# Optimization experiments

Hardware: AMD Instinct MI355X
Metric: run time of the kernel (lower is better)

## Reference

```python
import jax, jax.numpy as jnp
import numpy as np

B, N, F, F_, H = 4, 2048, 64, 64, 4
EDGE_PROB = 0.01  # sparsity of the random adjacency


def setup_inputs() -> dict:
    key = jax.random.key(0)
    k_x, k_a, k_ws, k_wn, k_as, k_an = jax.random.split(key, 6)
    X = jax.random.normal(k_x, (B, N, F), dtype=jnp.float32)
    # binary adjacency with self-loops (float, as in the torch module)
    A = (jax.random.uniform(k_a, (B, N, N)) < EDGE_PROB).astype(jnp.float32)
    A = jnp.maximum(A, jnp.eye(N, dtype=jnp.float32)[None, :, :])
    # glorot-uniform-like init scale for [F, F_] kernels
    lim_k = np.sqrt(6.0 / (F + F_)).astype(np.float32)
    lim_a = np.sqrt(6.0 / (F_ + 1)).astype(np.float32)
    W_self = jax.random.uniform(k_ws, (H, F, F_), minval=-lim_k, maxval=lim_k, dtype=jnp.float32)
    W_neigh = jax.random.uniform(k_wn, (H, F, F_), minval=-lim_k, maxval=lim_k, dtype=jnp.float32)
    a_self = jax.random.uniform(k_as, (H, F_), minval=-lim_a, maxval=lim_a, dtype=jnp.float32)
    a_neigh = jax.random.uniform(k_an, (H, F_), minval=-lim_a, maxval=lim_a, dtype=jnp.float32)
    return {"X": X, "A": A, "W_self": W_self, "W_neigh": W_neigh,
            "a_self": a_self, "a_neigh": a_neigh}


def reference(X, A, W_self, W_neigh, a_self, a_neigh):
    # per-head linear projections: [B,H,N,F_]
    feat_self = jnp.einsum('bnf,hfe->bhne', X, W_self)
    feat_neigh = jnp.einsum('bnf,hfe->bhne', X, W_neigh)
    # scalar attention logits per node: [B,H,N]
    s_self = jnp.einsum('bhne,he->bhn', feat_self, a_self)
    s_neigh = jnp.einsum('bhne,he->bhn', feat_neigh, a_neigh)
    # pairwise logits: att[b,h,i,j] = s_self[b,h,i] + s_neigh[b,h,j]
    att = s_self[:, :, :, None] + s_neigh[:, :, None, :]
    att = jax.nn.leaky_relu(att, negative_slope=0.2)
    att = att + (-1e16) * (1.0 - A[:, None, :, :])  # additive adjacency mask
    att = jax.nn.sigmoid(att)
    att_sum = jnp.sum(att, axis=-1, keepdims=True)      # [B,H,N,1]
    inv = 1.0 / (1.0 + att_sum)
    att = att * inv                                      # sigmoid-normalized
    beta_promoter = inv
    # aggregate: self contribution scaled by beta + neighbor aggregation
    node_feat = feat_self * beta_promoter + jnp.einsum('bhnm,bhme->bhne', att, feat_neigh)
    # concat heads -> [B,N,H*F_], then ReLU activation
    out = jnp.transpose(node_feat, (0, 2, 1, 3)).reshape(X.shape[0], X.shape[1], -1)
    out = jax.nn.relu(out)
    return out, att
```

## Files before the change

### kernel.cpp

```cpp
#include <hip/hip_runtime.h>
#include <hip/hip_bf16.h>
#include <math.h>

constexpr int Bc = 4;
constexpr int Nc = 2048;
constexpr int Fc = 64;
constexpr int Hc = 4;

typedef float f32x4 __attribute__((ext_vector_type(4)));

__device__ __forceinline__ float readlane_f(float v, int l) {
    return __int_as_float(__builtin_amdgcn_readlane(__float_as_int(v), l));
}

__global__ __launch_bounds__(256) void proj_kernel(
    const float* __restrict__ X,
    const float* __restrict__ Wself, const float* __restrict__ Wneigh,
    const float* __restrict__ aSelf, const float* __restrict__ aNeigh,
    float* __restrict__ fS, float* __restrict__ fN,
    float* __restrict__ sS, float* __restrict__ sN)
{
    const int lane = threadIdx.x & 63;
    const int wave = threadIdx.x >> 6;
    const int ntiles = Nc / 64;
    const int tile = blockIdx.x % ntiles;
    const int bh   = blockIdx.x / ntiles;
    const int h = bh % Hc;
    const int b = bh / Hc;

    float wSr[64], wNr[64];
    const float* wsb = Wself  + (size_t)h * Fc * Fc + lane;
    const float* wnb = Wneigh + (size_t)h * Fc * Fc + lane;
#pragma unroll
    for (int f = 0; f < 64; ++f) {
        wSr[f] = wsb[f * 64];
        wNr[f] = wnb[f * 64];
    }
    const float aSe = aSelf[h * Fc + lane];
    const float aNe = aNeigh[h * Fc + lane];

    for (int ni = 0; ni < 16; ++ni) {
        const int n = tile * 64 + wave * 16 + ni;
        const float x = X[((size_t)b * Nc + n) * Fc + lane];
        float accS = 0.f, accN = 0.f;
#pragma unroll
        for (int f = 0; f < 64; ++f) {
            const float xf = readlane_f(x, f);
            accS = fmaf(xf, wSr[f], accS);
            accN = fmaf(xf, wNr[f], accN);
        }
        const size_t row = (size_t)(b * Hc + h) * Nc + n;
        fS[row * Fc + lane] = accS;
        fN[row * Fc + lane] = accN;

        float rs = accS * aSe, rn = accN * aNe;
#pragma unroll
        for (int o = 32; o > 0; o >>= 1) {
            rs += __shfl_xor(rs, o, 64);
            rn += __shfl_xor(rn, o, 64);
        }
        if (lane == 0) { sS[row] = rs; sN[row] = rn; }
    }
}

__global__ __launch_bounds__(256) void att_kernel(
    const float* __restrict__ A,
    const float* __restrict__ sS, const float* __restrict__ sN,
    const float* __restrict__ fS, const float* __restrict__ fN,
    float* __restrict__ out, float* __restrict__ att)
{
    const int lane = threadIdx.x & 63;
    const int wave = threadIdx.x >> 6;
    const int row  = blockIdx.x * 4 + wave;
    const int b = row >> 11;
    const int i = row & (Nc - 1);

    const f32x4* Arow4 = (const f32x4*)(A + ((size_t)b * Nc + i) * Nc);
    f32x4 a4[8];
#pragma unroll
    for (int k = 0; k < 8; ++k)
        a4[k] = __builtin_nontemporal_load(&Arow4[k * 64 + lane]);

    for (int h = 0; h < Hc; ++h) {
        const size_t plane = (size_t)(b * Hc + h) * Nc;
        const float ssh = sS[plane + i];
        const float* sNh = sN + plane;

        f32x4 sig4[8];
        float lsum = 0.f;
#pragma unroll
        for (int k = 0; k < 8; ++k) {
#pragma unroll
            for (int c = 0; c < 4; ++c) {
                float sg = 0.f;
                if (a4[k][c] != 0.f) {
                    const int j = (k * 64 + lane) * 4 + c;
                    float z = ssh + sNh[j];
                    z = z > 0.f ? z : 0.2f * z;
                    sg = 1.f / (1.f + __expf(-z));
                }
                sig4[k][c] = sg;
                lsum += sg;
            }
        }
#pragma unroll
        for (int o = 32; o > 0; o >>= 1) lsum += __shfl_xor(lsum, o, 64);
        const float inv = 1.f / (1.f + lsum);

        f32x4* dst = (f32x4*)(att + (plane + i) * (size_t)Nc);
#pragma unroll
        for (int k = 0; k < 8; ++k) {
            f32x4 vv = sig4[k] * inv;
            __builtin_nontemporal_store(vv, &dst[k * 64 + lane]);
        }

        float acc = fS[(plane + i) * Fc + lane];
#pragma unroll
        for (int k = 0; k < 8; ++k) {
#pragma unroll
            for (int c = 0; c < 4; ++c) {
                unsigned long long m = __ballot(sig4[k][c] != 0.f);
                while (m) {
                    const int src = __builtin_ctzll(m);
                    m &= m - 1;
                    const int j = (k * 64 + src) * 4 + c;
                    const float w = __shfl(sig4[k][c], src, 64);
                    acc = fmaf(w, fN[(plane + j) * Fc + lane], acc);
                }
            }
        }
        acc *= inv;
        acc = acc > 0.f ? acc : 0.f;
        out[((size_t)b * Nc + i) * (Hc * Fc) + h * Fc + lane] = acc;
    }
}

extern "C" void kernel_launch(void* const* d_in, const int* in_sizes, int n_in,
                              void* d_out, int out_size, void* d_ws, size_t ws_size,
                              hipStream_t stream) {
    const float* X      = (const float*)d_in[0];
    const float* A      = (const float*)d_in[1];
    const float* Wself  = (const float*)d_in[2];
    const float* Wneigh = (const float*)d_in[3];
    const float* aSelf  = (const float*)d_in[4];
    const float* aNeigh = (const float*)d_in[5];

    float* out = (float*)d_out;
    float* att = out + (size_t)Bc * Nc * Hc * Fc;

    float* ws = (float*)d_ws;
    float* fS = ws;
    float* fN = fS + (size_t)Bc * Hc * Nc * Fc;
    float* sS = fN + (size_t)Bc * Hc * Nc * Fc;
    float* sN = sS + (size_t)Bc * Hc * Nc;

    proj_kernel<<<Bc * Hc * (Nc / 64), 256, 0, stream>>>(
        X, Wself, Wneigh, aSelf, aNeigh, fS, fN, sS, sN);
    att_kernel<<<(Bc * Nc) / 4, 256, 0, stream>>>(
        A, sS, sN, fS, fN, out, att);
}
```

Baseline: 406.7 us.

## Compact neighbor lists in LDS and process all heads per row together

Each wave compacts a row's nonzero adjacency entries into a shared-memory index list via ballot/prefix counts, then computes sigmoid weights for all four heads at once. The neighbor logits are stored interleaved by head so a single vector load fetches all heads. Aggregation gathers fN rows in batches of eight to increase memory-level parallelism, replacing the serial ballot/shuffle loop. Blocks are remapped so batch index varies fastest. A fallback path keeps the old per-head loop when a row has more than CAP neighbors, at the cost of extra LDS use and code size.

New measurement: 362.4 us. 10.9% less time.

```diff
diff --git a/kernel.cpp b/kernel.cpp
--- a/kernel.cpp
+++ b/kernel.cpp
@@ -6,6 +6,7 @@
 constexpr int Nc = 2048;
 constexpr int Fc = 64;
 constexpr int Hc = 4;
+constexpr int CAP = 128;
 
 typedef float f32x4 __attribute__((ext_vector_type(4)));
 
@@ -18,7 +19,7 @@
     const float* __restrict__ Wself, const float* __restrict__ Wneigh,
     const float* __restrict__ aSelf, const float* __restrict__ aNeigh,
     float* __restrict__ fS, float* __restrict__ fN,
-    float* __restrict__ sS, float* __restrict__ sN)
+    float* __restrict__ sS, float* __restrict__ sNt)
 {
     const int lane = threadIdx.x & 63;
     const int wave = threadIdx.x >> 6;
@@ -59,21 +60,27 @@
             rs += __shfl_xor(rs, o, 64);
             rn += __shfl_xor(rn, o, 64);
         }
-        if (lane == 0) { sS[row] = rs; sN[row] = rn; }
+        if (lane == 0) {
+            sS[row] = rs;
+            sNt[((size_t)b * Nc + n) * Hc + h] = rn;
+        }
     }
 }
 
 __global__ __launch_bounds__(256) void att_kernel(
     const float* __restrict__ A,
-    const float* __restrict__ sS, const float* __restrict__ sN,
+    const float* __restrict__ sS, const float* __restrict__ sNt,
     const float* __restrict__ fS, const float* __restrict__ fN,
     float* __restrict__ out, float* __restrict__ att)
 {
+    __shared__ int   idx_s[4][CAP + 8];
+    __shared__ f32x4 w_s[4][CAP + 8];
+
     const int lane = threadIdx.x & 63;
     const int wave = threadIdx.x >> 6;
-    const int row  = blockIdx.x * 4 + wave;
-    const int b = row >> 11;
-    const int i = row & (Nc - 1);
+    const int b = blockIdx.x & 3;
+    const int i = (blockIdx.x >> 2) * 4 + wave;
+    const f32x4 zero4 = {0.f, 0.f, 0.f, 0.f};
 
     const f32x4* Arow4 = (const f32x4*)(A + ((size_t)b * Nc + i) * Nc);
     f32x4 a4[8];
@@ -81,57 +88,164 @@
     for (int k = 0; k < 8; ++k)
         a4[k] = __builtin_nontemporal_load(&Arow4[k * 64 + lane]);
 
-    for (int h = 0; h < Hc; ++h) {
-        const size_t plane = (size_t)(b * Hc + h) * Nc;
-        const float ssh = sS[plane + i];
-        const float* sNh = sN + plane;
-
-        f32x4 sig4[8];
-        float lsum = 0.f;
+    float ss4[Hc];
+#pragma unroll
+    for (int h = 0; h < Hc; ++h) ss4[h] = sS[((size_t)(b * Hc + h)) * Nc + i];
+
+    const f32x4* sNt4 = (const f32x4*)(sNt + (size_t)b * Nc * Hc);
+
+    int cnt = 0;
+    unsigned posb[8] = {0, 0, 0, 0, 0, 0, 0, 0};
+#pragma unroll
+    for (int k = 0; k < 8; ++k) {
+#pragma unroll
+        for (int c = 0; c < 4; ++c) {
+            const bool act = a4[k][c] != 0.f;
+            const unsigned long long m = __ballot(act);
+            if (m) {
+                const int pre = (int)__popcll(m & ((1ull << lane) - 1ull));
+                const int pos = cnt + pre;
+                if (act) {
+                    posb[k] |= (unsigned)(pos & 255) << (8 * c);
+                    if (pos < CAP) idx_s[wave][pos] = (k * 64 + lane) * 4 + c;
+                }
+                cnt += (int)__popcll(m);
+            }
+        }
+    }
+
+    if (cnt <= CAP) {
+        if (lane < 8) idx_s[wave][cnt + lane] = i;
+
+        f32x4 sigr0 = zero4, sigr1 = zero4;
+        float sum4[Hc] = {0.f, 0.f, 0.f, 0.f};
+        if (lane < cnt) {
+            const int j = idx_s[wave][lane];
+            const f32x4 sn4 = sNt4[j];
+#pragma unroll
+            for (int h = 0; h < Hc; ++h) {
+                float z = ss4[h] + sn4[h];
+                z = z > 0.f ? z : 0.2f * z;
+                const float sg = 1.f / (1.f + __expf(-z));
+                sigr0[h] = sg; sum4[h] += sg;
+            }
+        }
+        if (cnt > 64) {
+            if (64 + lane < cnt) {
+                const int j = idx_s[wave][64 + lane];
+                const f32x4 sn4 = sNt4[j];
+#pragma unroll
+                for (int h = 0; h < Hc; ++h) {
+                    float z = ss4[h] + sn4[h];
+                    z = z > 0.f ? z : 0.2f * z;
+                    const float sg = 1.f / (1.f + __expf(-z));
+                    sigr1[h] = sg; sum4[h] += sg;
+                }
+            }
+        }
+#pragma unroll
+        for (int o = 32; o > 0; o >>= 1)
+#pragma unroll
+            for (int h = 0; h < Hc; ++h) sum4[h] += __shfl_xor(sum4[h], o, 64);
+        f32x4 inv4;
+#pragma unroll
+        for (int h = 0; h < Hc; ++h) inv4[h] = 1.f / (1.f + sum4[h]);
+
+        if (lane < cnt) w_s[wave][lane] = sigr0 * inv4;
+        if (cnt > 64 && 64 + lane < cnt) w_s[wave][64 + lane] = sigr1 * inv4;
+        if (lane < 8) w_s[wave][cnt + lane] = zero4;
+
 #pragma unroll
         for (int k = 0; k < 8; ++k) {
+            f32x4 wc[4];
 #pragma unroll
             for (int c = 0; c < 4; ++c) {
-                float sg = 0.f;
-                if (a4[k][c] != 0.f) {
-                    const int j = (k * 64 + lane) * 4 + c;
-                    float z = ssh + sNh[j];
-                    z = z > 0.f ? z : 0.2f * z;
-                    sg = 1.f / (1.f + __expf(-z));
-                }
-                sig4[k][c] = sg;
-                lsum += sg;
-            }
-        }
-#pragma unroll
-        for (int o = 32; o > 0; o >>= 1) lsum += __shfl_xor(lsum, o, 64);
-        const float inv = 1.f / (1.f + lsum);
-
-        f32x4* dst = (f32x4*)(att + (plane + i) * (size_t)Nc);
-#pragma unroll
-        for (int k = 0; k < 8; ++k) {
-            f32x4 vv = sig4[k] * inv;
-            __builtin_nontemporal_store(vv, &dst[k * 64 + lane]);
-        }
-
-        float acc = fS[(plane + i) * Fc + lane];
-#pragma unroll
-        for (int k = 0; k < 8; ++k) {
-#pragma unroll
-            for (int c = 0; c < 4; ++c) {
-                unsigned long long m = __ballot(sig4[k][c] != 0.f);
-                while (m) {
-                    const int src = __builtin_ctzll(m);
-                    m &= m - 1;
-                    const int j = (k * 64 + src) * 4 + c;
-                    const float w = __shfl(sig4[k][c], src, 64);
-                    acc = fmaf(w, fN[(plane + j) * Fc + lane], acc);
-                }
-            }
-        }
-        acc *= inv;
-        acc = acc > 0.f ? acc : 0.f;
-        out[((size_t)b * Nc + i) * (Hc * Fc) + h * Fc + lane] = acc;
+                const int pos = (posb[k] >> (8 * c)) & 255;
+                wc[c] = (a4[k][c] != 0.f) ? w_s[wave][pos] : zero4;
+            }
+#pragma unroll
+            for (int h = 0; h < Hc; ++h) {
+                f32x4 sg = {wc[0][h], wc[1][h], wc[2][h], wc[3][h]};
+                f32x4* dst = (f32x4*)(att + (((size_t)(b * Hc + h)) * Nc + i) * (size_t)Nc);
+                __builtin_nontemporal_store(sg, &dst[k * 64 + lane]);
+            }
+        }
+
+        f32x4 accv;
+#pragma unroll
+        for (int h = 0; h < Hc; ++h)
+            accv[h] = fS[(((size_t)(b * Hc + h)) * Nc + i) * Fc + lane] * inv4[h];
+        for (int base = 0; base < cnt; base += 8) {
+            int jv[8];
+#pragma unroll
+            for (int u = 0; u < 8; ++u) jv[u] = idx_s[wave][base + u];
+#pragma unroll
+            for (int h = 0; h < Hc; ++h) {
+                float wv[8], xv[8];
+#pragma unroll
+                for (int u = 0; u < 8; ++u) wv[u] = w_s[wave][base + u][h];
+#pragma unroll
+                for (int u = 0; u < 8; ++u)
+                    xv[u] = fN[(((size_t)(b * Hc + h)) * Nc + jv[u]) * Fc + lane];
+#pragma unroll
+                for (int u = 0; u < 8; ++u) accv[h] = fmaf(wv[u], xv[u], accv[h]);
+            }
+        }
+#pragma unroll
+        for (int h = 0; h < Hc; ++h) {
+            const float r = accv[h] > 0.f ? accv[h] : 0.f;
+            out[((size_t)b * Nc + i) * (Hc * Fc) + h * Fc + lane] = r;
+        }
+    } else {
+        for (int h = 0; h < Hc; ++h) {
+            const size_t plane = (size_t)(b * Hc + h) * Nc;
+            f32x4 sig4[8];
+            float lsum = 0.f;
+#pragma unroll
+            for (int k = 0; k < 8; ++k) {
+#pragma unroll
+                for (int c = 0; c < 4; ++c) {
+                    float sg = 0.f;
+                    if (a4[k][c] != 0.f) {
+                        const int j = (k * 64 + lane) * 4 + c;
+                        float z = ss4[h] + sNt[((size_t)b * Nc + j) * Hc + h];
+                        z = z > 0.f ? z : 0.2f * z;
+                        sg = 1.f / (1.f + __expf(-z));
+                    }
+                    sig4[k][c] = sg;
+                    lsum += sg;
+                }
+            }
+#pragma unroll
+            for (int o = 32; o > 0; o >>= 1) lsum += __shfl_xor(lsum, o, 64);
+            const float inv = 1.f / (1.f + lsum);
+
+            f32x4* dst = (f32x4*)(att + (plane + i) * (size_t)Nc);
+#pragma unroll
+            for (int k = 0; k < 8; ++k) {
+                f32x4 vv = sig4[k] * inv;
+                __builtin_nontemporal_store(vv, &dst[k * 64 + lane]);
+            }
+
+            float acc = fS[(plane + i) * Fc + lane];
+#pragma unroll
+            for (int k = 0; k < 8; ++k) {
+#pragma unroll
+                for (int c = 0; c < 4; ++c) {
+                    unsigned long long m = __ballot(sig4[k][c] != 0.f);
+                    while (m) {
+                        const int src = __builtin_ctzll(m);
+                        m &= m - 1;
+                        const int j = (k * 64 + src) * 4 + c;
+                        const float w = __shfl(sig4[k][c], src, 64);
+                        acc = fmaf(w, fN[(plane + j) * Fc + lane], acc);
+                    }
+                }
+            }
+            acc *= inv;
+            acc = acc > 0.f ? acc : 0.f;
+            out[((size_t)b * Nc + i) * (Hc * Fc) + h * Fc + lane] = acc;
+        }
     }
 }
 
@@ -149,13 +263,13 @@
     float* att = out + (size_t)Bc * Nc * Hc * Fc;
 
     float* ws = (float*)d_ws;
-    float* fS = ws;
-    float* fN = fS + (size_t)Bc * Hc * Nc * Fc;
-    float* sS = fN + (size_t)Bc * Hc * Nc * Fc;
-    float* sN = sS + (size_t)Bc * Hc * Nc;
+    float* fS  = ws;
+    float* fN  = fS + (size_t)Bc * Hc * Nc * Fc;
+    float* sS  = fN + (size_t)Bc * Hc * Nc * Fc;
+    float* sNt = sS + (size_t)Bc * Hc * Nc;
 
     proj_kernel<<<Bc * Hc * (Nc / 64), 256, 0, stream>>>(
-        X, Wself, Wneigh, aSelf, aNeigh, fS, fN, sS, sN);
+        X, Wself, Wneigh, aSelf, aNeigh, fS, fN, sS, sNt);
     att_kernel<<<(Bc * Nc) / 4, 256, 0, stream>>>(
-        A, sS, sN, fS, fN, out, att);
-}
+        A, sS, sNt, fS, fN, out, att);
+}
```
